# Performance work log

Hardware: AMD Instinct MI355X
Metric: run time of the kernel (lower is better)

## Reference

```python
import jax, jax.numpy as jnp
import numpy as np

NEG_SLOPE = 0.2  # PyG GATConv default leaky_relu slope


def gat_layer(x, W, a_src, a_dst, b):
    # x: [B, N, Fin]; W: [Fin, H*C]; a_src/a_dst: [H, C]; b: [H*C]
    # Dense-block equivalent of PyG GATConv on a fully-connected block graph
    # (self loops included), concat=True.
    B, N, Fin = x.shape
    H, C = a_src.shape
    h = jnp.einsum('bnf,fhc->bnhc', x, W.reshape(Fin, H, C))  # [B,N,H,C]
    ls = jnp.einsum('bnhc,hc->bnh', h, a_src)  # alpha_src per node
    ld = jnp.einsum('bnhc,hc->bnh', h, a_dst)  # alpha_dst per node
    # logits[i, j] = leaky_relu(alpha_dst[i] + alpha_src[j]); softmax over j
    logits = jax.nn.leaky_relu(ld[:, :, None, :] + ls[:, None, :, :], NEG_SLOPE)  # [B,i,j,H]
    attn = jax.nn.softmax(logits, axis=2)
    out = jnp.einsum('bijh,bjhc->bihc', attn, h).reshape(B, N, H * C)
    return out + b


def setup_inputs() -> dict:
    key = jax.random.key(0)
    ks = jax.random.split(key, 12)
    bs, R, Nc, enc = 8, 256, 64, 31
    H, hid, out = 8, 64, 32
    Fin = 1 + enc  # 32
    p = lambda k, shape: jax.random.normal(k, shape, jnp.float32) * 0.05
    return {
        'xs': jax.random.normal(ks[0], (bs, R, Nc), jnp.float32),
        'pos_enc': jax.random.normal(ks[1], (bs, Nc, enc), jnp.float32),
        'W1': p(ks[2], (Fin, H * hid)), 'as1': p(ks[3], (H, hid)), 'ad1': p(ks[4], (H, hid)),
        'b1': jnp.zeros((H * hid,), jnp.float32),
        'W2': p(ks[5], (H * hid, H * hid)), 'as2': p(ks[6], (H, hid)), 'ad2': p(ks[7], (H, hid)),
        'b2': jnp.zeros((H * hid,), jnp.float32),
        'W3': p(ks[8], (H * hid, H * out)), 'as3': p(ks[9], (H, out)), 'ad3': p(ks[10], (H, out)),
        'b3': jnp.zeros((H * out,), jnp.float32),
    }


def reference(xs, pos_enc, W1, as1, ad1, b1, W2, as2, ad2, b2, W3, as3, ad3, b3):
    bs, R, Nc = xs.shape
    enc = pos_enc.shape[-1]
    pe = jnp.broadcast_to(pos_enc[:, None], (bs, R, Nc, enc))
    x = jnp.concatenate([xs[..., None], pe], axis=-1)  # [bs,R,Nc,1+enc]
    x = x.reshape(bs * R, Nc, 1 + enc)  # independent fully-connected blocks
    x = gat_layer(x, W1, as1, ad1, b1)
    x = gat_layer(x, W2, as2, ad2, b2)
    x = gat_layer(x, W3, as3, ad3, b3)
    out = x.reshape(bs, R, Nc, -1).mean(axis=2)  # mean over num_xs
    return out
```

## Files before the change

### kernel.cpp

```cpp
#include <hip/hip_runtime.h>
#include <hip/hip_bf16.h>

typedef __hip_bfloat16 bf16;
typedef unsigned int uint32;
typedef __attribute__((ext_vector_type(8))) short short8;
typedef __attribute__((ext_vector_type(4))) float float4v;
typedef __attribute__((ext_vector_type(16))) float float16v;

#define THREADS 512
#define LDX 520
#define LDE 68
#define LOG2E 1.44269504088896340736f

__device__ __forceinline__ bf16 f2b(float x) { return __float2bfloat16(x); }
__device__ __forceinline__ uint32 packbf2(float x, float y) {
  union { __hip_bfloat162 b; uint32 u; } cv;
  cv.b = __float22bfloat162_rn(make_float2(x, y));
  return cv.u;
}
__device__ __forceinline__ bf16 f2b1(float x) {
  union { uint32 u; unsigned short s[2]; } cv;
  cv.u = packbf2(x, x);
  union { unsigned short s; bf16 b; } r;
  r.s = cv.s[0];
  return r.b;
}
__device__ __forceinline__ float exp2_hw(float x) {
#if __has_builtin(__builtin_amdgcn_exp2f)
  return __builtin_amdgcn_exp2f(x);
#else
  float r;
  asm("v_exp_f32 %0, %1" : "=v"(r) : "v"(x));
  return r;
#endif
}
__device__ __forceinline__ float rcp_hw(float x) {
#if __has_builtin(__builtin_amdgcn_rcpf)
  return __builtin_amdgcn_rcpf(x);
#else
  float r;
  asm("v_rcp_f32 %0, %1" : "=v"(r) : "v"(x));
  return r;
#endif
}
__device__ __forceinline__ void lane32_swap(uint32 a, uint32 b, int q,
                                            uint32& lo, uint32& hi) {
#if __has_builtin(__builtin_amdgcn_permlane32_swap)
  auto r = __builtin_amdgcn_permlane32_swap(a, b, false, false);
  lo = r[0];
  hi = r[1];
  (void)q;
#else
  uint32 pa = (uint32)__shfl_xor((int)a, 32, 64);
  uint32 pb = (uint32)__shfl_xor((int)b, 32, 64);
  lo = q ? pb : a;
  hi = q ? b : pa;
#endif
}

__global__ void convw_all(const float* __restrict__ W1,
                          const float* __restrict__ W2,
                          const float* __restrict__ W3, bf16* __restrict__ dst) {
  int o = blockIdx.x * 256 + threadIdx.x;
  if (o >= 409600) return;
  const float* W;
  int Mlog, loc;
  if (o < 16384) { W = W1; Mlog = 9; loc = o; }
  else if (o < 278528) { W = W2; Mlog = 9; loc = o - 16384; }
  else { W = W3; Mlog = 8; loc = o - 278528; }
  int j = loc & 7, q = (loc >> 3) & 1, rest = loc >> 4;
  int M = 1 << Mlog;
  int n = rest & (M - 1), kb = rest >> Mlog;
  int k = kb * 16 + q * 8 + j;
  dst[o] = f2b(W[(size_t)k * M + n]);
}

__global__ void convE_all(
    const float* __restrict__ W1, const float* __restrict__ as1, const float* __restrict__ ad1,
    const float* __restrict__ W2, const float* __restrict__ as2, const float* __restrict__ ad2,
    const float* __restrict__ W3, const float* __restrict__ as3, const float* __restrict__ ad3,
    bf16* __restrict__ dstE) {
  int o = blockIdx.x * 256 + threadIdx.x;
  if (o >= 16896) return;
  const float *W, *as_, *ad_;
  int M, C, loc;
  if (o < 512) { loc = o; W = W1; as_ = as1; ad_ = ad1; M = 512; C = 64; }
  else if (o < 8704) { loc = o - 512; W = W2; as_ = as2; ad_ = ad2; M = 512; C = 64; }
  else { loc = o - 8704; W = W3; as_ = as3; ad_ = ad3; M = 256; C = 32; }
  int j = loc & 7, kc = (loc >> 3) & 3, n = (loc >> 5) & 15, ks = loc >> 9;
  int k = ks * 32 + kc * 8 + j;
  int head = n & 7;
  const float* a = (n < 8) ? as_ : ad_;
  float s = 0.f;
  for (int c = 0; c < C; ++c)
    s += W[(size_t)k * M + head * C + c] * a[head * C + c];
  dstE[o] = f2b(s * LOG2E);
}

template <int K, int M, int C, bool LAST>
__device__ __forceinline__ void gat_layer(
    int t, const bf16* __restrict__ Wswz, const bf16* __restrict__ WE,
    const float* __restrict__ bias, bf16* sX, float* sE) {
  constexpr int NCT = C / 32;
  constexpr int KS16 = K / 16;
  constexpr int KSE = K / 32;
  const int lane = t & 63;
  const int hu = __builtin_amdgcn_readfirstlane(t >> 6);
  const int c = lane & 31, q = lane >> 5;
  const int ln16 = lane & 15, kq16 = lane >> 4;
  const int colbase = hu * C;

  if (hu < 4) {
    float4v acce = (float4v)0.f;
#pragma unroll
    for (int ks = 0; ks < KSE; ++ks) {
      short8 afrE = *(const short8*)(sX + (hu * 16 + ln16) * LDX + ks * 32 + kq16 * 8);
      short8 efr = *(const short8*)(WE + ks * 512 + ln16 * 32 + kq16 * 8);
      acce = __builtin_amdgcn_mfma_f32_16x16x32_bf16(afrE, efr, acce, 0, 0, 0);
    }
    *(float4v*)(sE + ln16 * LDE + hu * 16 + kq16 * 4) = acce;
  }

  uint32 Ppk[NCT][4][4];
  {
    float16v acc[2][NCT];
#pragma unroll
    for (int rt = 0; rt < 2; ++rt)
#pragma unroll
      for (int ct = 0; ct < NCT; ++ct) acc[rt][ct] = (float16v)0.f;
    const bf16* ap = sX + c * LDX + q * 8;
    const bf16* bp = Wswz + ((colbase + c) * 2 + q) * 8;
#pragma unroll 4
    for (int ks = 0; ks < KS16; ++ks) {
      short8 afr[2];
      afr[0] = *(const short8*)(ap + ks * 16);
      afr[1] = *(const short8*)(ap + 32 * LDX + ks * 16);
      short8 bfr[NCT];
#pragma unroll
      for (int ct = 0; ct < NCT; ++ct)
        bfr[ct] = *(const short8*)(bp + (size_t)ks * (M * 16) + ct * 32 * 16);
#pragma unroll
      for (int rt = 0; rt < 2; ++rt)
#pragma unroll
        for (int ct = 0; ct < NCT; ++ct)
          acc[rt][ct] = __builtin_amdgcn_mfma_f32_32x32x16_bf16(
              afr[rt], bfr[ct], acc[rt][ct], 0, 0, 0);
    }
#pragma unroll
    for (int rt = 0; rt < 2; ++rt)
#pragma unroll
      for (int ct = 0; ct < NCT; ++ct)
#pragma unroll
        for (int tp = 0; tp < 2; ++tp) {
          Ppk[ct][rt * 2 + tp][0] = packbf2(acc[rt][ct][8 * tp + 0], acc[rt][ct][8 * tp + 1]);
          Ppk[ct][rt * 2 + tp][1] = packbf2(acc[rt][ct][8 * tp + 2], acc[rt][ct][8 * tp + 3]);
          Ppk[ct][rt * 2 + tp][2] = packbf2(acc[rt][ct][8 * tp + 4], acc[rt][ct][8 * tp + 5]);
          Ppk[ct][rt * 2 + tp][3] = packbf2(acc[rt][ct][8 * tp + 6], acc[rt][ct][8 * tp + 7]);
        }
  }

  __syncthreads();

  const float* lsrow = sE + hu * LDE;
  const float* ldrow = sE + (8 + hu) * LDE;
  short8 pfr[2][4];
#pragma unroll
  for (int rt = 0; rt < 2; ++rt) {
    const float ldi = ldrow[rt * 32 + c];
    float pe_[4][8];
    float rsum = 0.f;
#pragma unroll
    for (int tt = 0; tt < 4; ++tt) {
      float4 v0 = *(const float4*)(lsrow + tt * 16 + q * 8);
      float4 v1 = *(const float4*)(lsrow + tt * 16 + q * 8 + 4);
      float ls8[8] = {v0.x, v0.y, v0.z, v0.w, v1.x, v1.y, v1.z, v1.w};
#pragma unroll
      for (int jj = 0; jj < 8; ++jj) {
        float tv = ldi + ls8[jj];
        float e = exp2_hw(fmaxf(tv, 0.2f * tv));
        pe_[tt][jj] = e;
        rsum += e;
      }
    }
    rsum += __shfl_xor(rsum, 32, 64);
    const float ri = rcp_hw(rsum);
#pragma unroll
    for (int tt = 0; tt < 4; ++tt) {
      union { uint32 d[4]; short8 s; } w;
#pragma unroll
      for (int jp = 0; jp < 4; ++jp)
        w.d[jp] = packbf2(pe_[tt][2 * jp] * ri, pe_[tt][2 * jp + 1] * ri);
      pfr[rt][tt] = w.s;
    }
  }

#pragma unroll
  for (int ct = 0; ct < NCT; ++ct) {
    short8 hfr[4];
#pragma unroll
    for (int tt = 0; tt < 4; ++tt) {
      uint32 U0 = Ppk[ct][tt][0], U1 = Ppk[ct][tt][1];
      uint32 V0 = Ppk[ct][tt][2], V1 = Ppk[ct][tt][3];
      uint32 d0, d1, d2, d3;
      lane32_swap(U0, V0, q, d0, d2);
      lane32_swap(U1, V1, q, d1, d3);
      union { uint32 d[4]; short8 s; } u;
      u.d[0] = d0; u.d[1] = d1; u.d[2] = d2; u.d[3] = d3;
      hfr[tt] = u.s;
    }
    float16v oacc[2];
    oacc[0] = (float16v)0.f;
    oacc[1] = (float16v)0.f;
#pragma unroll
    for (int tt = 0; tt < 4; ++tt) {
      oacc[0] = __builtin_amdgcn_mfma_f32_32x32x16_bf16(pfr[0][tt], hfr[tt], oacc[0], 0, 0, 0);
      oacc[1] = __builtin_amdgcn_mfma_f32_32x32x16_bf16(pfr[1][tt], hfr[tt], oacc[1], 0, 0, 0);
    }
    const float bv = bias[colbase + ct * 32 + c];
#pragma unroll
    for (int rt = 0; rt < 2; ++rt)
#pragma unroll
      for (int r = 0; r < 16; ++r) {
        float val = oacc[rt][r] + bv;
        int row = rt * 32 + (r & 3) + 8 * (r >> 2) + 4 * q;
        if constexpr (LAST)
          ((float*)sX)[row * 260 + colbase + ct * 32 + c] = val;
        else
          sX[row * LDX + colbase + ct * 32 + c] = f2b1(val);
      }
  }
  __syncthreads();
}

__global__ __launch_bounds__(THREADS, 4) void gat3_mfma(
    const float* __restrict__ xs, const float* __restrict__ pe,
    const bf16* __restrict__ W1s, const bf16* __restrict__ WE1,
    const float* __restrict__ b1, const bf16* __restrict__ W2s,
    const bf16* __restrict__ WE2, const float* __restrict__ b2,
    const bf16* __restrict__ W3s, const bf16* __restrict__ WE3,
    const float* __restrict__ b3, float* __restrict__ out) {
  extern __shared__ char smem[];
  bf16* sX = (bf16*)smem;
  float* sE = (float*)(smem + 66560);

  const int t = threadIdx.x;
  const int blk = blockIdx.x;
  const int bidx = blk >> 8;

  for (int idx = t; idx < 64 * 32; idx += THREADS) {
    int n = idx >> 5, f = idx & 31;
    float v = (f == 0) ? xs[blk * 64 + n] : pe[(bidx * 64 + n) * 31 + (f - 1)];
    sX[n * LDX + f] = f2b(v);
  }
  __syncthreads();

  gat_layer<32, 512, 64, false>(t, W1s, WE1, b1, sX, sE);
  gat_layer<512, 512, 64, false>(t, W2s, WE2, b2, sX, sE);
  gat_layer<512, 256, 32, true>(t, W3s, WE3, b3, sX, sE);

  const float* xf = (const float*)sX;
  if (t < 256) {
    float s = 0.f;
#pragma unroll 8
    for (int i = 0; i < 64; ++i) s += xf[i * 260 + t];
    out[blk * 256 + t] = s * 0.015625f;
  }
}

extern "C" void kernel_launch(void* const* d_in, const int* in_sizes, int n_in,
                              void* d_out, int out_size, void* d_ws, size_t ws_size,
                              hipStream_t stream) {
  const float* xs = (const float*)d_in[0];
  const float* pe = (const float*)d_in[1];
  const float* W1 = (const float*)d_in[2];
  const float* as1 = (const float*)d_in[3];
  const float* ad1 = (const float*)d_in[4];
  const float* b1 = (const float*)d_in[5];
  const float* W2 = (const float*)d_in[6];
  const float* as2 = (const float*)d_in[7];
  const float* ad2 = (const float*)d_in[8];
  const float* b2 = (const float*)d_in[9];
  const float* W3 = (const float*)d_in[10];
  const float* as3 = (const float*)d_in[11];
  const float* ad3 = (const float*)d_in[12];
  const float* b3 = (const float*)d_in[13];

  bf16* Wall = (bf16*)d_ws;
  bf16* WEall = Wall + 409600;
  bf16* W1s = Wall;
  bf16* W2s = Wall + 16384;
  bf16* W3s = Wall + 278528;
  bf16* WE1 = WEall;
  bf16* WE2 = WEall + 512;
  bf16* WE3 = WEall + 8704;

  convw_all<<<dim3(1600), dim3(256), 0, stream>>>(W1, W2, W3, Wall);
  convE_all<<<dim3(66), dim3(256), 0, stream>>>(W1, as1, ad1, W2, as2, ad2,
                                                W3, as3, ad3, WEall);

  const size_t smem = 70912;
  (void)hipFuncSetAttribute((const void*)gat3_mfma,
                            hipFuncAttributeMaxDynamicSharedMemorySize,
                            (int)smem);
  gat3_mfma<<<dim3(2048), dim3(THREADS), smem, stream>>>(
      xs, pe, W1s, WE1, b1, W2s, WE2, b2, W3s, WE3, b3, (float*)d_out);
}
```

Measured before the change: 243.0 us.

## Merge weight prep kernels, coalesce reads, and raise wave priority around MFMAs

Fuses the two weight-preprocessing kernels into one launch. The bf16 swizzle now reads W coalesced and scatters the writes, and the attention-projection precompute uses one wave per input row with vector loads and a shuffle reduction instead of serial strided loops. It also wraps the MFMA blocks in the main kernel with s_setprio to favour matrix issue over other waves. These remove a launch and a slow serial prep step; the priority hints could disturb how waves interleave.

```diff
diff --git a/kernel.cpp b/kernel.cpp
--- a/kernel.cpp
+++ b/kernel.cpp
@@ -58,43 +58,65 @@
 #endif
 }
 
-__global__ void convw_all(const float* __restrict__ W1,
-                          const float* __restrict__ W2,
-                          const float* __restrict__ W3, bf16* __restrict__ dst) {
-  int o = blockIdx.x * 256 + threadIdx.x;
-  if (o >= 409600) return;
-  const float* W;
-  int Mlog, loc;
-  if (o < 16384) { W = W1; Mlog = 9; loc = o; }
-  else if (o < 278528) { W = W2; Mlog = 9; loc = o - 16384; }
-  else { W = W3; Mlog = 8; loc = o - 278528; }
-  int j = loc & 7, q = (loc >> 3) & 1, rest = loc >> 4;
-  int M = 1 << Mlog;
-  int n = rest & (M - 1), kb = rest >> Mlog;
-  int k = kb * 16 + q * 8 + j;
-  dst[o] = f2b(W[(size_t)k * M + n]);
-}
-
-__global__ void convE_all(
-    const float* __restrict__ W1, const float* __restrict__ as1, const float* __restrict__ ad1,
-    const float* __restrict__ W2, const float* __restrict__ as2, const float* __restrict__ ad2,
-    const float* __restrict__ W3, const float* __restrict__ as3, const float* __restrict__ ad3,
-    bf16* __restrict__ dstE) {
-  int o = blockIdx.x * 256 + threadIdx.x;
-  if (o >= 16896) return;
+__global__ void prep_all(const float* __restrict__ W1, const float* __restrict__ W2,
+                         const float* __restrict__ W3,
+                         const float* __restrict__ as1, const float* __restrict__ ad1,
+                         const float* __restrict__ as2, const float* __restrict__ ad2,
+                         const float* __restrict__ as3, const float* __restrict__ ad3,
+                         bf16* __restrict__ dst, bf16* __restrict__ dstE) {
+  const int b = blockIdx.x;
+  const int t = threadIdx.x;
+  if (b < 1600) {
+    int o = b * 256 + t;
+    const float* W;
+    int Mlog, loc, dbase;
+    if (o < 16384) { W = W1; Mlog = 9; loc = o; dbase = 0; }
+    else if (o < 278528) { W = W2; Mlog = 9; loc = o - 16384; dbase = 16384; }
+    else { W = W3; Mlog = 8; loc = o - 278528; dbase = 278528; }
+    float v = W[loc];
+    int M = 1 << Mlog;
+    int n = loc & (M - 1), k = loc >> Mlog;
+    int kb = k >> 4, q = (k >> 3) & 1, j = k & 7;
+    dst[dbase + ((kb * M + n) * 2 + q) * 8 + j] = f2b(v);
+    return;
+  }
+  const int kr = (b - 1600) * 4 + (t >> 6);
+  const int l = t & 63;
   const float *W, *as_, *ad_;
-  int M, C, loc;
-  if (o < 512) { loc = o; W = W1; as_ = as1; ad_ = ad1; M = 512; C = 64; }
-  else if (o < 8704) { loc = o - 512; W = W2; as_ = as2; ad_ = ad2; M = 512; C = 64; }
-  else { loc = o - 8704; W = W3; as_ = as3; ad_ = ad3; M = 256; C = 32; }
-  int j = loc & 7, kc = (loc >> 3) & 3, n = (loc >> 5) & 15, ks = loc >> 9;
-  int k = ks * 32 + kc * 8 + j;
-  int head = n & 7;
-  const float* a = (n < 8) ? as_ : ad_;
-  float s = 0.f;
-  for (int c = 0; c < C; ++c)
-    s += W[(size_t)k * M + head * C + c] * a[head * C + c];
-  dstE[o] = f2b(s * LOG2E);
+  int M, lk, dbase;
+  if (kr < 32)       { W = W1; as_ = as1; ad_ = ad1; M = 512; lk = kr;       dbase = 0; }
+  else if (kr < 544) { W = W2; as_ = as2; ad_ = ad2; M = 512; lk = kr - 32;  dbase = 512; }
+  else               { W = W3; as_ = as3; ad_ = ad3; M = 256; lk = kr - 544; dbase = 8704; }
+  const float* wr = W + (size_t)lk * M;
+  float ps = 0.f, pd = 0.f;
+  if (M == 512) {
+    float4 w0 = *(const float4*)(wr + 8 * l);
+    float4 w1 = *(const float4*)(wr + 8 * l + 4);
+    float4 s0 = *(const float4*)(as_ + 8 * l);
+    float4 s1 = *(const float4*)(as_ + 8 * l + 4);
+    float4 d0 = *(const float4*)(ad_ + 8 * l);
+    float4 d1 = *(const float4*)(ad_ + 8 * l + 4);
+    ps = w0.x * s0.x + w0.y * s0.y + w0.z * s0.z + w0.w * s0.w +
+         w1.x * s1.x + w1.y * s1.y + w1.z * s1.z + w1.w * s1.w;
+    pd = w0.x * d0.x + w0.y * d0.y + w0.z * d0.z + w0.w * d0.w +
+         w1.x * d1.x + w1.y * d1.y + w1.z * d1.z + w1.w * d1.w;
+  } else {
+    float4 w0 = *(const float4*)(wr + 4 * l);
+    float4 s0 = *(const float4*)(as_ + 4 * l);
+    float4 d0 = *(const float4*)(ad_ + 4 * l);
+    ps = w0.x * s0.x + w0.y * s0.y + w0.z * s0.z + w0.w * s0.w;
+    pd = w0.x * d0.x + w0.y * d0.y + w0.z * d0.z + w0.w * d0.w;
+  }
+#pragma unroll
+  for (int m = 1; m < 8; m <<= 1) {
+    ps += __shfl_xor(ps, m, 64);
+    pd += __shfl_xor(pd, m, 64);
+  }
+  const int j = lk & 7, kc = (lk >> 3) & 3, ks = lk >> 5;
+  const int h = l >> 3;
+  const int base = dbase + ks * 512 + kc * 8 + j;
+  if ((l & 7) == 0) dstE[base + h * 32] = f2b(ps * LOG2E);
+  if ((l & 7) == 1) dstE[base + (8 + h) * 32] = f2b(pd * LOG2E);
 }
 
 template <int K, int M, int C, bool LAST>
@@ -116,7 +138,9 @@
     for (int ks = 0; ks < KSE; ++ks) {
       short8 afrE = *(const short8*)(sX + (hu * 16 + ln16) * LDX + ks * 32 + kq16 * 8);
       short8 efr = *(const short8*)(WE + ks * 512 + ln16 * 32 + kq16 * 8);
+      __builtin_amdgcn_s_setprio(1);
       acce = __builtin_amdgcn_mfma_f32_16x16x32_bf16(afrE, efr, acce, 0, 0, 0);
+      __builtin_amdgcn_s_setprio(0);
     }
     *(float4v*)(sE + ln16 * LDE + hu * 16 + kq16 * 4) = acce;
   }
@@ -139,12 +163,14 @@
 #pragma unroll
       for (int ct = 0; ct < NCT; ++ct)
         bfr[ct] = *(const short8*)(bp + (size_t)ks * (M * 16) + ct * 32 * 16);
+      __builtin_amdgcn_s_setprio(1);
 #pragma unroll
       for (int rt = 0; rt < 2; ++rt)
 #pragma unroll
         for (int ct = 0; ct < NCT; ++ct)
           acc[rt][ct] = __builtin_amdgcn_mfma_f32_32x32x16_bf16(
               afr[rt], bfr[ct], acc[rt][ct], 0, 0, 0);
+      __builtin_amdgcn_s_setprio(0);
     }
 #pragma unroll
     for (int rt = 0; rt < 2; ++rt)
@@ -211,11 +237,13 @@
     float16v oacc[2];
     oacc[0] = (float16v)0.f;
     oacc[1] = (float16v)0.f;
+    __builtin_amdgcn_s_setprio(1);
 #pragma unroll
     for (int tt = 0; tt < 4; ++tt) {
       oacc[0] = __builtin_amdgcn_mfma_f32_32x32x16_bf16(pfr[0][tt], hfr[tt], oacc[0], 0, 0, 0);
       oacc[1] = __builtin_amdgcn_mfma_f32_32x32x16_bf16(pfr[1][tt], hfr[tt], oacc[1], 0, 0, 0);
     }
+    __builtin_amdgcn_s_setprio(0);
     const float bv = bias[colbase + ct * 32 + c];
 #pragma unroll
     for (int rt = 0; rt < 2; ++rt)
@@ -294,9 +322,8 @@
   bf16* WE2 = WEall + 512;
   bf16* WE3 = WEall + 8704;
 
-  convw_all<<<dim3(1600), dim3(256), 0, stream>>>(W1, W2, W3, Wall);
-  convE_all<<<dim3(66), dim3(256), 0, stream>>>(W1, as1, ad1, W2, as2, ad2,
-                                                W3, as3, ad3, WEall);
+  prep_all<<<dim3(1864), dim3(256), 0, stream>>>(
+      W1, W2, W3, as1, ad1, as2, ad2, as3, ad3, Wall, WEall);
 
   const size_t smem = 70912;
   (void)hipFuncSetAttribute((const void*)gat3_mfma,
```

Measured after the change: 244.7 us. No clear change (+0.7%).
